# Kernel tuning notes

Hardware: AMD Instinct MI355X
Metric: run time of the kernel (lower is better)

Reference implementation:

```python
import jax, jax.numpy as jnp
import numpy as np

B, N, P, H, E, M, O, T = 16, 64, 192, 64, 32, 64, 64, 256

def _mlp(x, W1, b1, W2, b2):
    return jax.nn.relu(x @ W1 + b1) @ W2 + b2

def _qmul(q, r):
    w1, x1, y1, z1 = q[..., 0], q[..., 1], q[..., 2], q[..., 3]
    w2, x2, y2, z2 = r[..., 0], r[..., 1], r[..., 2], r[..., 3]
    return jnp.stack([
        w1*w2 - x1*x2 - y1*y2 - z1*z2,
        w1*x2 + x1*w2 + y1*z2 - z1*y2,
        w1*y2 - x1*z2 + y1*w2 + z1*x2,
        w1*z2 + x1*y2 - y1*x2 + z1*w2], axis=-1)

def _qrot(q, v):
    # rotate vector v by unit quaternion q (w,x,y,z)
    qv = q[..., 1:]
    t = 2.0 * jnp.cross(qv, v)
    return v + q[..., :1] * t + jnp.cross(qv, t)

def _normalize(x):
    return x / jnp.maximum(jnp.linalg.norm(x, axis=-1, keepdims=True), 1e-12)

def _lin(k, i, o, s=0.05):
    return jax.random.normal(k, (i, o), jnp.float32) * s

def setup_inputs():
    key = jax.random.key(0)
    ks = jax.random.split(key, 24)
    return dict(
        peptide_quats=_normalize(jax.random.normal(ks[0], (B, N, 4), jnp.float32)),
        peptide_trans=jax.random.normal(ks[1], (B, N, 3), jnp.float32) * 10.0,
        peptide_torsions=_normalize(jax.random.normal(ks[2], (B, N, 7, 2), jnp.float32)),
        peptide_feats=jax.random.normal(ks[3], (B, N, H), jnp.float32),
        edge_feats=jax.random.normal(ks[4], (B, N, N, E), jnp.float32),
        pocket_feats=jax.random.normal(ks[5], (B, P, H), jnp.float32),
        pocket_quats=_normalize(jax.random.normal(ks[6], (B, P, 4), jnp.float32)),
        pocket_trans=jax.random.normal(ks[7], (B, P, 3), jnp.float32) * 10.0,
        Wm1=_lin(ks[8], 2*H + E + 9, T), bm1=jnp.zeros((T,), jnp.float32),
        Wm2=_lin(ks[9], T, M), bm2=jnp.zeros((M,), jnp.float32),
        Wf1=_lin(ks[10], H + M, T), bf1=jnp.zeros((T,), jnp.float32),
        Wf2=_lin(ks[11], T, O), bf2=jnp.zeros((O,), jnp.float32),
        Wt1=_lin(ks[12], M, T), bt1=jnp.zeros((T,), jnp.float32),
        Wt2=_lin(ks[13], T, 3), bt2=jnp.zeros((3,), jnp.float32),
        Wq1=_lin(ks[14], M, T), bq1=jnp.zeros((T,), jnp.float32),
        Wq2=_lin(ks[15], T, 4), bq2=jnp.zeros((4,), jnp.float32),
        Wo1=_lin(ks[16], M + 14, T), bo1=jnp.zeros((T,), jnp.float32),
        Wo2=_lin(ks[17], T, 14), bo2=jnp.zeros((14,), jnp.float32),
        peptide_mask=jnp.ones((B, N), bool),
        pocket_mask=jnp.ones((B, P), bool),
    )

def reference(peptide_quats, peptide_trans, peptide_torsions, peptide_feats, edge_feats,
              pocket_feats, pocket_quats, pocket_trans,
              Wm1, bm1, Wm2, bm2, Wf1, bf1, Wf2, bf2, Wt1, bt1, Wt2, bt2,
              Wq1, bq1, Wq2, bq2, Wo1, bo1, Wo2, bo2, peptide_mask, pocket_mask):
    NP = N + P
    eye = jnp.eye(N, dtype=bool)
    pep_mm = peptide_mask[..., :, None] & peptide_mask[..., None, :] & ~eye
    poc_mm = peptide_mask[..., :, None] & pocket_mask[..., None, :]
    mm = jnp.concatenate([pep_mm, poc_mm], axis=-1)  # [B,N,N+P]

    all_q = jnp.concatenate([peptide_quats, pocket_quats], axis=-2)  # [B,N+P,4]
    all_x = jnp.concatenate([peptide_trans, pocket_trans], axis=-2)  # [B,N+P,3]

    conj = jnp.asarray([1.0, -1.0, -1.0, -1.0], peptide_quats.dtype)
    q_inv = all_q * conj                 # inverse rotation (unit quats)
    t_inv = -_qrot(q_inv, all_x)         # inverse translation

    # express peptide position i in the local frame of neighbour j
    local_x = _qrot(q_inv[..., None, :, :], peptide_trans[..., :, None, :]) + t_inv[..., None, :, :]
    local_q = _qmul(q_inv[..., None, :, :], peptide_quats[..., :, None, :])
    d2 = jnp.sum(jnp.square(peptide_trans[..., :, None, :] - all_x[..., None, :, :]), axis=-1)
    qdot = jnp.abs(jnp.sum(peptide_quats[..., :, None, :] * all_q[..., None, :, :], axis=-1))

    h_i = jnp.broadcast_to(peptide_feats[..., :, None, :], (B, N, NP, H))
    all_h = jnp.concatenate([peptide_feats, pocket_feats], axis=-2)
    h_j = jnp.broadcast_to(all_h[..., None, :, :], (B, N, NP, H))
    e = jnp.concatenate([edge_feats, jnp.zeros((B, N, P, E), edge_feats.dtype)], axis=-2)

    msg_in = jnp.concatenate([h_i, h_j, e, local_x, local_q, d2[..., None], qdot[..., None]], axis=-1)
    message = _mlp(msg_in, Wm1, bm1, Wm2, bm2) * mm[..., None]
    msg_sum = message.sum(axis=-2)  # [B,N,M]

    o = _mlp(jnp.concatenate([peptide_feats, msg_sum], axis=-1), Wf1, bf1, Wf2, bf2)

    n_msg = mm.sum(axis=-1).astype(message.dtype)
    c = jnp.where(n_msg > 0, 1.0 / jnp.maximum(n_msg, 1.0), 0.0)
    has_msg = n_msg > 0

    # translation update (rotate per-edge delta from neighbour local to global frame)
    delta_x = _mlp(message, Wt1, bt1, Wt2, bt2) * mm[..., None]
    rotated = _qrot(all_q[..., None, :, :], delta_x)
    upd_x = peptide_trans + rotated.sum(axis=-2) * c[..., None]

    # rotation update
    dq = _normalize(_mlp(msg_sum * c[..., None], Wq1, bq1, Wq2, bq2))
    upd_q = jnp.where(has_msg[..., None], _qmul(peptide_quats, dq), peptide_quats)
    upd_q = _normalize(upd_q)  # Rigid(..., normalize_quats=True)

    # torsion update (angle addition in sin/cos form)
    flat_t = peptide_torsions.reshape(B, N, 14)
    dt = _mlp(jnp.concatenate([msg_sum * c[..., None], flat_t], axis=-1), Wo1, bo1, Wo2, bo2)
    dt = _normalize(dt.reshape(B, N, 7, 2))
    s1, c1 = peptide_torsions[..., 0], peptide_torsions[..., 1]
    s2, c2 = dt[..., 0], dt[..., 1]
    mult = jnp.stack([s1 * c2 + c1 * s2, c1 * c2 - s1 * s2], axis=-1)
    upd_t = jnp.where(has_msg[..., None, None], mult, peptide_torsions)

    return upd_q, upd_x, upd_t, o
```

## Files before the change

### kernel.cpp

```cpp
#include <hip/hip_runtime.h>


typedef _Float16 f16;
typedef f16 f16x8 __attribute__((ext_vector_type(8)));
typedef f16 f16x4 __attribute__((ext_vector_type(4)));
typedef float f32x4 __attribute__((ext_vector_type(4)));
#define MFMA16(a, b, c) __builtin_amdgcn_mfma_f32_16x16x32_f16(a, b, c, 0, 0, 0)

#define B_ 16
#define N_ 64
#define P_ 192
#define NP_ 256
#define H_ 64
#define T_ 256

#define OFF_HIA    0
#define OFF_HJB    262144
#define OFF_B1T    1379328
#define OFF_W2T    1387520
#define OFF_WT1H   1395712
#define OFF_W1AT   1403904
#define OFF_W1BT   1412096

#define OUT_UPDQ 0
#define OUT_UPDX 4096
#define OUT_UPDT 7168
#define OUT_O    21504

__device__ __forceinline__ void qrot(float qw, float qx, float qy, float qz,
                                     float vx, float vy, float vz,
                                     float& ox, float& oy, float& oz) {
    float tx = 2.f * (qy * vz - qz * vy);
    float ty = 2.f * (qz * vx - qx * vz);
    float tz = 2.f * (qx * vy - qy * vx);
    ox = vx + qw * tx + (qy * tz - qz * ty);
    oy = vy + qw * ty + (qz * tx - qx * tz);
    oz = vz + qw * tz + (qx * ty - qy * tx);
}

struct Wts {
    const float *Wm1,*bm1,*Wm2,*bm2,*Wf1,*bf1,*Wf2,*bf2,*Wt1,*bt1,*Wt2,*bt2,
                *Wq1,*bq1,*Wq2,*bq2,*Wo1,*bo1,*Wo2,*bo2;
};

__global__ __launch_bounds__(256) void k_prep(const float* __restrict__ Wm1,
                                              const float* __restrict__ Wm2,
                                              const float* __restrict__ Wt1,
                                              float* __restrict__ ws) {
    int t = blockIdx.x * 256 + threadIdx.x;
    if (t < 16384) {
        f16* B1T = (f16*)(ws + OFF_B1T);
        int c = t >> 6, k = t & 63;
        float v = 0.f;
        if (k < 32) v = Wm1[(128 + k) * 256 + c];
        else if (k < 41) v = Wm1[(160 + (k - 32)) * 256 + c];
        B1T[t] = (f16)v;
    } else if (t < 32768) {
        f16* W2T = (f16*)(ws + OFF_W2T);
        int u = t - 16384;
        int m = u >> 8, c = u & 255;
        W2T[u] = (f16)Wm2[c * 64 + m];
    } else if (t < 49152) {
        f16* W1H = (f16*)(ws + OFF_WT1H);
        int u = t - 32768;
        int c = u >> 6, m = u & 63;
        W1H[u] = (f16)Wt1[m * 256 + c];
    } else if (t < 65536) {
        f16* W1A = (f16*)(ws + OFF_W1AT);
        int u = t - 49152;
        int c = u >> 6, k = u & 63;
        W1A[u] = (f16)Wm1[k * 256 + c];
    } else {
        f16* W1B = (f16*)(ws + OFF_W1BT);
        int u = t - 65536;
        int c = u >> 6, k = u & 63;
        W1B[u] = (f16)Wm1[(64 + k) * 256 + c];
    }
}

__global__ __launch_bounds__(256) void k_dots(const float* __restrict__ pep_h,
                                              const float* __restrict__ poc_h,
                                              float* __restrict__ ws) {
    const int ct = blockIdx.x;
    const int b = blockIdx.y;
    const int tid = threadIdx.x;
    const int lane = tid & 63;
    const int wv = tid >> 6;
    const int lm = lane & 15;
    const int lq = lane >> 4;

    __shared__ __align__(16) f16 hL[256 * 64];

    {
        const float4* p4 = (const float4*)(pep_h + (size_t)b * 4096);
        #pragma unroll
        for (int it = 0; it < 4; it++) {
            int idx = it * 256 + tid;
            float4 v = p4[idx];
            f16x4 h = {(f16)v.x, (f16)v.y, (f16)v.z, (f16)v.w};
            *(f16x4*)&hL[idx * 4] = h;
        }
        const float4* q4 = (const float4*)(poc_h + (size_t)b * 12288);
        #pragma unroll
        for (int it = 0; it < 12; it++) {
            int idx = it * 256 + tid;
            float4 v = q4[idx];
            f16x4 h = {(f16)v.x, (f16)v.y, (f16)v.z, (f16)v.w};
            *(f16x4*)&hL[4096 + idx * 4] = h;
        }
    }
    __syncthreads();

    const f16* W1AT = (const f16*)(ws + OFF_W1AT);
    const f16* W1BT = (const f16*)(ws + OFF_W1BT);

    f32x4 acc[4][4];
    #pragma unroll
    for (int mt = 0; mt < 4; mt++)
        #pragma unroll
        for (int nt = 0; nt < 4; nt++) acc[mt][nt] = (f32x4){0.f, 0.f, 0.f, 0.f};

    f16x8 af[4][2], bf[4][2];
    #pragma unroll
    for (int mt = 0; mt < 4; mt++) {
        const int c = ct * 64 + mt * 16 + lm;
        af[mt][0] = *(const f16x8*)&W1BT[c * 64 + lq * 8];
        af[mt][1] = *(const f16x8*)&W1BT[c * 64 + 32 + lq * 8];
    }
    #pragma unroll
    for (int nt = 0; nt < 4; nt++) {
        const int jj = wv * 64 + nt * 16 + lm;
        bf[nt][0] = *(const f16x8*)&hL[jj * 64 + lq * 8];
        bf[nt][1] = *(const f16x8*)&hL[jj * 64 + 32 + lq * 8];
    }
    #pragma unroll
    for (int mt = 0; mt < 4; mt++)
        #pragma unroll
        for (int nt = 0; nt < 4; nt++) {
            acc[mt][nt] = MFMA16(af[mt][0], bf[nt][0], acc[mt][nt]);
            acc[mt][nt] = MFMA16(af[mt][1], bf[nt][1], acc[mt][nt]);
        }
    float* HJ = ws + OFF_HJB + (size_t)b * 65536;
    #pragma unroll
    for (int mt = 0; mt < 4; mt++)
        #pragma unroll
        for (int nt = 0; nt < 4; nt++)
            #pragma unroll
            for (int r = 0; r < 4; r++)
                HJ[(size_t)(ct * 64 + mt * 16 + lq * 4 + r) * 256 +
                   wv * 64 + nt * 16 + lm] = acc[mt][nt][r];

    f32x4 ha[4];
    #pragma unroll
    for (int nt = 0; nt < 4; nt++) ha[nt] = (f32x4){0.f, 0.f, 0.f, 0.f};
    f16x8 a0 = *(const f16x8*)&hL[(wv * 16 + lm) * 64 + lq * 8];
    f16x8 a1 = *(const f16x8*)&hL[(wv * 16 + lm) * 64 + 32 + lq * 8];
    #pragma unroll
    for (int nt = 0; nt < 4; nt++) {
        const int c = ct * 64 + nt * 16 + lm;
        f16x8 b0 = *(const f16x8*)&W1AT[c * 64 + lq * 8];
        f16x8 b1 = *(const f16x8*)&W1AT[c * 64 + 32 + lq * 8];
        ha[nt] = MFMA16(a0, b0, ha[nt]);
        ha[nt] = MFMA16(a1, b1, ha[nt]);
    }
    #pragma unroll
    for (int nt = 0; nt < 4; nt++)
        #pragma unroll
        for (int r = 0; r < 4; r++)
            ws[OFF_HIA + (size_t)(b * 64 + wv * 16 + lq * 4 + r) * 256 +
               ct * 64 + nt * 16 + lm] = ha[nt][r];
}

__global__ __launch_bounds__(256, 2) void k_edge(const float* __restrict__ pep_q,
                                                 const float* __restrict__ pep_x,
                                                 const float* __restrict__ pep_t,
                                                 const float* __restrict__ pep_h,
                                                 const float* __restrict__ ef,
                                                 const float* __restrict__ poc_q,
                                                 const float* __restrict__ poc_x,
                                                 Wts W, float* __restrict__ ws,
                                                 float* __restrict__ out) {
    const int b = blockIdx.x & 15;
    const int i = blockIdx.x >> 4;
    const int node = b * 64 + i;
    const int tid = threadIdx.x;
    const int j = tid;
    const int lane = tid & 63;
    const int wv = tid >> 6;
    const int lm = lane & 15;
    const int lq = lane >> 4;
    const int j0w = wv * 64;
    const float cfac = 1.f / 255.f;

    __shared__ __align__(16) unsigned char RAW[45056];
    __shared__ float base_s[256], bt1s[256], wt2s[768];
    __shared__ float bm2s[64];
    __shared__ float msump[4][64];
    __shared__ float rotp[4][3];
    __shared__ float MS_s[64], MSC_s[64], ROT_s[3], DQ_s[4], DT_s[14];

    f16* const A1 = (f16*)RAW;
    f16* const Tw = (f16*)(RAW + 24576 + wv * 5120);
    float* const DXb = (float*)(RAW + 24576 + wv * 5120 + 2048);

    base_s[tid] = ws[OFF_HIA + (size_t)node * T_ + tid] + W.bm1[tid];
    bt1s[tid] = W.bt1[tid];
    if (tid < 64) bm2s[tid] = W.bm2[tid];
    wt2s[tid]       = W.Wt2[tid];
    wt2s[256 + tid] = W.Wt2[256 + tid];
    wt2s[512 + tid] = W.Wt2[512 + tid];

    const bool pep = (j < N_);
    {
        const float4 qi4 = *reinterpret_cast<const float4*>(pep_q + (b * N_ + i) * 4);
        const float qiw = qi4.x, qix = qi4.y, qiy = qi4.z, qiz = qi4.w;
        const float* tip = pep_x + (b * N_ + i) * 3;
        const float tix = tip[0], tiy = tip[1], tiz = tip[2];

        float qjw, qjx, qjy, qjz, xjx, xjy, xjz;
        if (pep) {
            const float4 q4 = *reinterpret_cast<const float4*>(pep_q + (b * N_ + j) * 4);
            qjw = q4.x; qjx = q4.y; qjy = q4.z; qjz = q4.w;
            const float* xp = pep_x + (b * N_ + j) * 3;
            xjx = xp[0]; xjy = xp[1]; xjz = xp[2];
        } else {
            const float4 q4 = *reinterpret_cast<const float4*>(poc_q + (b * P_ + (j - N_)) * 4);
            qjw = q4.x; qjx = q4.y; qjy = q4.z; qjz = q4.w;
            const float* xp = poc_x + (b * P_ + (j - N_)) * 3;
            xjx = xp[0]; xjy = xp[1]; xjz = xp[2];
        }

        const float vw = qjw, vx = -qjx, vy = -qjy, vz = -qjz;
        float tnx, tny, tnz;
        qrot(vw, vx, vy, vz, xjx, xjy, xjz, tnx, tny, tnz);
        float lxx, lxy, lxz;
        qrot(vw, vx, vy, vz, tix, tiy, tiz, lxx, lxy, lxz);
        lxx -= tnx; lxy -= tny; lxz -= tnz;
        float lqw = vw * qiw - vx * qix - vy * qiy - vz * qiz;
        float lqx = vw * qix + vx * qiw + vy * qiz - vz * qiy;
        float lqy = vw * qiy - vx * qiz + vy * qiw + vz * qix;
        float lqz = vw * qiz + vx * qiy - vy * qix + vz * qiw;
        float ddx = tix - xjx, ddy = tiy - xjy, ddz = tiz - xjz;
        float d2 = ddx * ddx + ddy * ddy + ddz * ddz;
        float qd = fabsf(qiw * qjw + qix * qjx + qiy * qjy + qiz * qjz);

        f16* arow = &A1[j * 48];
        const f16x8 z = {(f16)0,(f16)0,(f16)0,(f16)0,(f16)0,(f16)0,(f16)0,(f16)0};
        if (pep) {
            const float4* ep = reinterpret_cast<const float4*>(
                ef + (size_t)(((b * N_ + i) * N_) + j) * 32);
            #pragma unroll
            for (int gr = 0; gr < 4; gr++) {
                float4 v0 = ep[gr * 2], v1 = ep[gr * 2 + 1];
                f16x8 h;
                h[0]=(f16)v0.x; h[1]=(f16)v0.y; h[2]=(f16)v0.z; h[3]=(f16)v0.w;
                h[4]=(f16)v1.x; h[5]=(f16)v1.y; h[6]=(f16)v1.z; h[7]=(f16)v1.w;
                *(f16x8*)(arow + gr * 8) = h;
            }
        } else {
            #pragma unroll
            for (int gr = 0; gr < 4; gr++) *(f16x8*)(arow + gr * 8) = z;
        }
        f16x8 hg;
        hg[0]=(f16)lxx; hg[1]=(f16)lxy; hg[2]=(f16)lxz; hg[3]=(f16)lqw;
        hg[4]=(f16)lqx; hg[5]=(f16)lqy; hg[6]=(f16)lqz; hg[7]=(f16)d2;
        *(f16x8*)(arow + 32) = hg;
        f16x8 h2 = z; h2[0] = (f16)qd;
        *(f16x8*)(arow + 40) = h2;
    }
    __syncthreads();

    const f16* B1Tg = (const f16*)(ws + OFF_B1T);
    const f16* W2Tg = (const f16*)(ws + OFF_W2T);
    const f16* W1Hg = (const f16*)(ws + OFF_WT1H);
    const float* hjb = ws + OFF_HJB + (size_t)b * 65536;

    f32x4 msgacc[4][4];
    #pragma unroll
    for (int mt = 0; mt < 4; mt++)
        #pragma unroll
        for (int nt = 0; nt < 4; nt++)
            msgacc[mt][nt] = (f32x4){0.f, 0.f, 0.f, 0.f};

    const f16x8 zf = {(f16)0,(f16)0,(f16)0,(f16)0,(f16)0,(f16)0,(f16)0,(f16)0};

    f16x8 g1c[2][2], g2c[4], g1n[2][2], g2n[4];
    #pragma unroll
    for (int nt = 0; nt < 2; nt++) {
        const int c = nt * 16 + lm;
        g1c[nt][0] = *(const f16x8*)&B1Tg[c * 64 + lq * 8];
        g1c[nt][1] = *(const f16x8*)&B1Tg[c * 64 + 32 + lq * 8];
    }
    #pragma unroll
    for (int nt = 0; nt < 4; nt++)
        g2c[nt] = *(const f16x8*)&W2Tg[(nt * 16 + lm) * 256 + lq * 8];

    for (int ch = 0; ch < 8; ch++) {
        const int c0 = ch * 32;
        if (ch < 7) {
            const int c1 = c0 + 32;
            #pragma unroll
            for (int nt = 0; nt < 2; nt++) {
                const int c = c1 + nt * 16 + lm;
                g1n[nt][0] = *(const f16x8*)&B1Tg[c * 64 + lq * 8];
                g1n[nt][1] = *(const f16x8*)&B1Tg[c * 64 + 32 + lq * 8];
            }
            #pragma unroll
            for (int nt = 0; nt < 4; nt++)
                g2n[nt] = *(const f16x8*)&W2Tg[(nt * 16 + lm) * 256 + c1 + lq * 8];
        }
        float4 hv[4][2];
        #pragma unroll
        for (int mt = 0; mt < 4; mt++)
            #pragma unroll
            for (int nt = 0; nt < 2; nt++) {
                const int c = c0 + nt * 16 + lm;
                hv[mt][nt] = *(const float4*)&hjb[(size_t)c * 256 + j0w + mt * 16 + lq * 4];
            }
        #pragma unroll
        for (int mt = 0; mt < 4; mt++) {
            const int jr = j0w + mt * 16 + lm;
            f16x8 a0 = *(const f16x8*)&A1[jr * 48 + lq * 8];
            f16x8 a1 = zf;
            if (lq < 2) a1 = *(const f16x8*)&A1[jr * 48 + 32 + lq * 8];
            #pragma unroll
            for (int nt = 0; nt < 2; nt++) {
                const int c = c0 + nt * 16 + lm;
                f32x4 acc = {0.f, 0.f, 0.f, 0.f};
                acc = MFMA16(a0, g1c[nt][0], acc);
                acc = MFMA16(a1, g1c[nt][1], acc);
                const int jl = mt * 16 + lq * 4;
                const float bc = base_s[c];
                const float* hvp = (const float*)&hv[mt][nt];
                #pragma unroll
                for (int r = 0; r < 4; r++) {
                    float u = acc[r] + hvp[r] + bc;
                    u = fmaxf(u, 0.f);
                    Tw[(jl + r) * 40 + nt * 16 + lm] = (f16)u;
                }
            }
        }
        __builtin_amdgcn_wave_barrier();
        #pragma unroll
        for (int mt = 0; mt < 4; mt++) {
            f16x8 a0 = *(const f16x8*)&Tw[(mt * 16 + lm) * 40 + lq * 8];
            #pragma unroll
            for (int nt = 0; nt < 4; nt++)
                msgacc[mt][nt] = MFMA16(a0, g2c[nt], msgacc[mt][nt]);
        }
        __builtin_amdgcn_wave_barrier();
        #pragma unroll
        for (int nt = 0; nt < 2; nt++) { g1c[nt][0] = g1n[nt][0]; g1c[nt][1] = g1n[nt][1]; }
        #pragma unroll
        for (int nt = 0; nt < 4; nt++) g2c[nt] = g2n[nt];
    }

    float sums[4] = {0.f, 0.f, 0.f, 0.f};
    #pragma unroll
    for (int mt = 0; mt < 4; mt++) {
        f16* bandrow = (mt < 3) ? (f16*)(RAW + wv * 6144 + (mt * 16) * 128)
                                : (f16*)(RAW + 24576 + wv * 5120);
        #pragma unroll
        for (int nt = 0; nt < 4; nt++) {
            const int m = nt * 16 + lm;
            f32x4 a = msgacc[mt][nt];
            #pragma unroll
            for (int r = 0; r < 4; r++) {
                const int jj = j0w + mt * 16 + lq * 4 + r;
                float v = a[r] + bm2s[m];
                if (jj == i) v = 0.f;
                bandrow[(lq * 4 + r) * 64 + m] = (f16)v;
                sums[nt] += v;
            }
        }
    }
    #pragma unroll
    for (int nt = 0; nt < 4; nt++) {
        float s = sums[nt];
        s += __shfl_xor(s, 16);
        s += __shfl_xor(s, 32);
        if (lane < 16) msump[wv][nt * 16 + lane] = s;
    }
    __syncthreads();
    if (tid < 64) {
        float s = msump[0][tid] + msump[1][tid] + msump[2][tid] + msump[3][tid];
        MS_s[tid] = s; MSC_s[tid] = s * cfac;
    }

    #pragma unroll
    for (int mt = 0; mt < 4; mt++) {
        const f16* mrow = (mt < 3)
            ? (const f16*)(RAW + wv * 6144 + (mt * 16 + lm) * 128)
            : (const f16*)(RAW + 24576 + wv * 5120 + lm * 128);
        f16x8 a0 = *(const f16x8*)&mrow[lq * 8];
        f16x8 a1 = *(const f16x8*)&mrow[32 + lq * 8];
        float d0[4] = {0,0,0,0}, d1[4] = {0,0,0,0}, d2a[4] = {0,0,0,0};
        #pragma unroll 8
        for (int nt = 0; nt < 16; nt++) {
            const int c = nt * 16 + lm;
            f16x8 b0 = *(const f16x8*)&W1Hg[c * 64 + lq * 8];
            f16x8 b1 = *(const f16x8*)&W1Hg[c * 64 + 32 + lq * 8];
            f32x4 acc = {0.f, 0.f, 0.f, 0.f};
            acc = MFMA16(a0, b0, acc);
            acc = MFMA16(a1, b1, acc);
            const float w0 = wt2s[c * 3 + 0];
            const float w1 = wt2s[c * 3 + 1];
            const float w2 = wt2s[c * 3 + 2];
            const float bc = bt1s[c];
            #pragma unroll
            for (int r = 0; r < 4; r++) {
                float s = fmaxf(acc[r] + bc, 0.f);
                d0[r] = fmaf(s, w0, d0[r]);
                d1[r] = fmaf(s, w1, d1[r]);
                d2a[r] = fmaf(s, w2, d2a[r]);
            }
        }
        #pragma unroll
        for (int r = 0; r < 4; r++) {
            float v0 = d0[r], v1 = d1[r], v2 = d2a[r];
            v0 += __shfl_xor(v0, 1); v0 += __shfl_xor(v0, 2);
            v0 += __shfl_xor(v0, 4); v0 += __shfl_xor(v0, 8);
            v1 += __shfl_xor(v1, 1); v1 += __shfl_xor(v1, 2);
            v1 += __shfl_xor(v1, 4); v1 += __shfl_xor(v1, 8);
            v2 += __shfl_xor(v2, 1); v2 += __shfl_xor(v2, 2);
            v2 += __shfl_xor(v2, 4); v2 += __shfl_xor(v2, 8);
            if (lm == 0) {
                const int jl = mt * 16 + lq * 4 + r;
                DXb[jl * 3 + 0] = v0;
                DXb[jl * 3 + 1] = v1;
                DXb[jl * 3 + 2] = v2;
            }
        }
    }

    float qjw, qjx, qjy, qjz;
    {
        const float* qp = pep ? (pep_q + (b * N_ + j) * 4)
                              : (poc_q + (b * P_ + (j - N_)) * 4);
        const float4 q4 = *reinterpret_cast<const float4*>(qp);
        qjw = q4.x; qjx = q4.y; qjy = q4.z; qjz = q4.w;
    }
    const float maskf = (pep && j == i) ? 0.f : 1.f;
    float dx0 = (DXb[lane * 3 + 0] + W.bt2[0]) * maskf;
    float dx1 = (DXb[lane * 3 + 1] + W.bt2[1]) * maskf;
    float dx2 = (DXb[lane * 3 + 2] + W.bt2[2]) * maskf;
    float rx, ry, rz;
    qrot(qjw, qjx, qjy, qjz, dx0, dx1, dx2, rx, ry, rz);
    {
        float v = rx;
        v += __shfl_xor(v, 32); v += __shfl_xor(v, 16); v += __shfl_xor(v, 8);
        v += __shfl_xor(v, 4);  v += __shfl_xor(v, 2);  v += __shfl_xor(v, 1);
        if (lane == 0) rotp[wv][0] = v;
        v = ry;
        v += __shfl_xor(v, 32); v += __shfl_xor(v, 16); v += __shfl_xor(v, 8);
        v += __shfl_xor(v, 4);  v += __shfl_xor(v, 2);  v += __shfl_xor(v, 1);
        if (lane == 0) rotp[wv][1] = v;
        v = rz;
        v += __shfl_xor(v, 32); v += __shfl_xor(v, 16); v += __shfl_xor(v, 8);
        v += __shfl_xor(v, 4);  v += __shfl_xor(v, 2);  v += __shfl_xor(v, 1);
        if (lane == 0) rotp[wv][2] = v;
    }
    __syncthreads();

    float* const FB = (float*)RAW;
    float* const HIS  = FB;
    float* const TORs = FB + 64;
    float* const HB   = FB + 128;
    float* const HB2  = FB + 384;
    float* const HB3  = FB + 640;

    if (tid >= 64 && tid < 67) {
        int k = tid - 64;
        ROT_s[k] = rotp[0][k] + rotp[1][k] + rotp[2][k] + rotp[3][k];
    }
    if (tid < 64) HIS[tid] = pep_h[(size_t)node * 64 + tid];
    if (tid >= 96 && tid < 110) TORs[tid - 96] = pep_t[(size_t)node * 14 + (tid - 96)];
    __syncthreads();

    {
        float acc = W.bf1[tid];
        #pragma unroll 16
        for (int k = 0; k < 64; k++) acc = fmaf(HIS[k], W.Wf1[k * 256 + tid], acc);
        #pragma unroll 16
        for (int k = 0; k < 64; k++) acc = fmaf(MS_s[k], W.Wf1[(64 + k) * 256 + tid], acc);
        HB[tid] = fmaxf(acc, 0.f);
    }
    __syncthreads();
    {
        float p = 0.f;
        #pragma unroll 16
        for (int c = 0; c < 64; c++)
            p = fmaf(HB[wv * 64 + c], W.Wf2[(wv * 64 + c) * 64 + lane], p);
        msump[wv][lane] = p;
    }
    {
        float acc = W.bq1[tid];
        #pragma unroll 16
        for (int k = 0; k < 64; k++) acc = fmaf(MSC_s[k], W.Wq1[k * 256 + tid], acc);
        HB2[tid] = fmaxf(acc, 0.f);
    }
    {
        float acc = W.bo1[tid];
        #pragma unroll 16
        for (int k = 0; k < 64; k++) acc = fmaf(MSC_s[k], W.Wo1[k * 256 + tid], acc);
        #pragma unroll
        for (int k = 0; k < 14; k++) acc = fmaf(TORs[k], W.Wo1[(64 + k) * 256 + tid], acc);
        HB3[tid] = fmaxf(acc, 0.f);
    }
    __syncthreads();
    if (tid < 64) {
        float o = W.bf2[tid] + msump[0][tid] + msump[1][tid] + msump[2][tid] + msump[3][tid];
        out[OUT_O + (size_t)node * 64 + tid] = o;
    }
    {
        float p = 0.f;
        #pragma unroll
        for (int t4 = 0; t4 < 4; t4++) {
            int c = t4 * 64 + lane;
            p = fmaf(HB2[c], W.Wq2[c * 4 + wv], p);
        }
        p += __shfl_xor(p, 32); p += __shfl_xor(p, 16); p += __shfl_xor(p, 8);
        p += __shfl_xor(p, 4);  p += __shfl_xor(p, 2);  p += __shfl_xor(p, 1);
        if (lane == 0) DQ_s[wv] = p + W.bq2[wv];
    }
    {
        const int g = tid >> 4, l16 = tid & 15;
        if (g < 14) {
            float p = 0.f;
            #pragma unroll
            for (int t16 = 0; t16 < 16; t16++) {
                int c = t16 * 16 + l16;
                p = fmaf(HB3[c], W.Wo2[c * 14 + g], p);
            }
            p += __shfl_xor(p, 8); p += __shfl_xor(p, 4);
            p += __shfl_xor(p, 2); p += __shfl_xor(p, 1);
            if (l16 == 0) DT_s[g] = p + W.bo2[g];
        }
    }
    __syncthreads();

    if (tid == 0) {
        float w_ = DQ_s[0], x_ = DQ_s[1], y_ = DQ_s[2], z_ = DQ_s[3];
        float n = fmaxf(sqrtf(w_ * w_ + x_ * x_ + y_ * y_ + z_ * z_), 1e-12f);
        w_ /= n; x_ /= n; y_ /= n; z_ /= n;
        const float4 qi4 = *reinterpret_cast<const float4*>(pep_q + (size_t)node * 4);
        float aw = qi4.x, ax = qi4.y, ay = qi4.z, az = qi4.w;
        float uw = aw * w_ - ax * x_ - ay * y_ - az * z_;
        float ux = aw * x_ + ax * w_ + ay * z_ - az * y_;
        float uy = aw * y_ - ax * z_ + ay * w_ + az * x_;
        float uz = aw * z_ + ax * y_ - ay * x_ + az * w_;
        float n2 = fmaxf(sqrtf(uw * uw + ux * ux + uy * uy + uz * uz), 1e-12f);
        out[OUT_UPDQ + (size_t)node * 4 + 0] = uw / n2;
        out[OUT_UPDQ + (size_t)node * 4 + 1] = ux / n2;
        out[OUT_UPDQ + (size_t)node * 4 + 2] = uy / n2;
        out[OUT_UPDQ + (size_t)node * 4 + 3] = uz / n2;
    }
    if (tid >= 32 && tid < 35) {
        int k = tid - 32;
        out[OUT_UPDX + (size_t)node * 3 + k] =
            pep_x[(size_t)node * 3 + k] + ROT_s[k] * cfac;
    }
    if (tid >= 48 && tid < 55) {
        int t = tid - 48;
        float s2 = DT_s[2 * t], c2 = DT_s[2 * t + 1];
        float n = fmaxf(sqrtf(s2 * s2 + c2 * c2), 1e-12f);
        s2 /= n; c2 /= n;
        float s1 = TORs[2 * t], c1 = TORs[2 * t + 1];
        out[OUT_UPDT + (size_t)node * 14 + 2 * t]     = s1 * c2 + c1 * s2;
        out[OUT_UPDT + (size_t)node * 14 + 2 * t + 1] = c1 * c2 - s1 * s2;
    }
}

extern "C" void kernel_launch(void* const* d_in, const int* in_sizes, int n_in,
                              void* d_out, int out_size, void* d_ws, size_t ws_size,
                              hipStream_t stream) {
    (void)in_sizes; (void)n_in; (void)out_size; (void)ws_size;
    const float* pep_q = (const float*)d_in[0];
    const float* pep_x = (const float*)d_in[1];
    const float* pep_t = (const float*)d_in[2];
    const float* pep_h = (const float*)d_in[3];
    const float* ef    = (const float*)d_in[4];
    const float* poc_h = (const float*)d_in[5];
    const float* poc_q = (const float*)d_in[6];
    const float* poc_x = (const float*)d_in[7];
    float* ws = (float*)d_ws;
    float* out = (float*)d_out;

    Wts W;
    W.Wm1 = (const float*)d_in[8];  W.bm1 = (const float*)d_in[9];
    W.Wm2 = (const float*)d_in[10]; W.bm2 = (const float*)d_in[11];
    W.Wf1 = (const float*)d_in[12]; W.bf1 = (const float*)d_in[13];
    W.Wf2 = (const float*)d_in[14]; W.bf2 = (const float*)d_in[15];
    W.Wt1 = (const float*)d_in[16]; W.bt1 = (const float*)d_in[17];
    W.Wt2 = (const float*)d_in[18]; W.bt2 = (const float*)d_in[19];
    W.Wq1 = (const float*)d_in[20]; W.bq1 = (const float*)d_in[21];
    W.Wq2 = (const float*)d_in[22]; W.bq2 = (const float*)d_in[23];
    W.Wo1 = (const float*)d_in[24]; W.bo1 = (const float*)d_in[25];
    W.Wo2 = (const float*)d_in[26]; W.bo2 = (const float*)d_in[27];

    k_prep<<<320, 256, 0, stream>>>(W.Wm1, W.Wm2, W.Wt1, ws);
    k_dots<<<dim3(4, 16), 256, 0, stream>>>(pep_h, poc_h, ws);
    k_edge<<<1024, 256, 0, stream>>>(pep_q, pep_x, pep_t, pep_h, ef,
                                     poc_q, poc_x, W, ws, out);
}
```

Measured before the change: 269.5 us.

## Use 512-thread blocks in k_edge with 32 edges per wave

Doubles the k_edge block to 8 waves, so each wave handles 32 neighbour edges instead of 64. The per-wave shared-memory scratch layout and the reductions are remapped to fit, and the node-level MLP tail is split across the two halves of the block. The aim is more waves in flight to hide latency and a shorter per-wave serial chain. In exchange, the weight fragments each wave loads from global memory are amortised over fewer edges, and the block needs more registers and barriers.

```diff
diff --git a/kernel.cpp b/kernel.cpp
--- a/kernel.cpp
+++ b/kernel.cpp
@@ -171,7 +171,7 @@
                ct * 64 + nt * 16 + lm] = ha[nt][r];
 }
 
-__global__ __launch_bounds__(256, 2) void k_edge(const float* __restrict__ pep_q,
+__global__ __launch_bounds__(512, 4) void k_edge(const float* __restrict__ pep_q,
                                                  const float* __restrict__ pep_x,
                                                  const float* __restrict__ pep_t,
                                                  const float* __restrict__ pep_h,
@@ -184,34 +184,35 @@
     const int i = blockIdx.x >> 4;
     const int node = b * 64 + i;
     const int tid = threadIdx.x;
-    const int j = tid;
     const int lane = tid & 63;
     const int wv = tid >> 6;
     const int lm = lane & 15;
     const int lq = lane >> 4;
-    const int j0w = wv * 64;
+    const int j0w = wv * 32;
     const float cfac = 1.f / 255.f;
 
     __shared__ __align__(16) unsigned char RAW[45056];
     __shared__ float base_s[256], bt1s[256], wt2s[768];
     __shared__ float bm2s[64];
-    __shared__ float msump[4][64];
-    __shared__ float rotp[4][3];
+    __shared__ float msump[8][64];
+    __shared__ float rotp[8][3];
     __shared__ float MS_s[64], MSC_s[64], ROT_s[3], DQ_s[4], DT_s[14];
 
     f16* const A1 = (f16*)RAW;
-    f16* const Tw = (f16*)(RAW + 24576 + wv * 5120);
-    float* const DXb = (float*)(RAW + 24576 + wv * 5120 + 2048);
-
-    base_s[tid] = ws[OFF_HIA + (size_t)node * T_ + tid] + W.bm1[tid];
-    bt1s[tid] = W.bt1[tid];
-    if (tid < 64) bm2s[tid] = W.bm2[tid];
-    wt2s[tid]       = W.Wt2[tid];
-    wt2s[256 + tid] = W.Wt2[256 + tid];
-    wt2s[512 + tid] = W.Wt2[512 + tid];
-
-    const bool pep = (j < N_);
-    {
+    f16* const Tw = (f16*)(RAW + 24576 + wv * 2560);
+    float* const DXb = (float*)(RAW + 24576 + wv * 2560 + 1024);
+
+    if (tid >= 256) {
+        const int t2 = tid - 256;
+        base_s[t2] = ws[OFF_HIA + (size_t)node * T_ + t2] + W.bm1[t2];
+        bt1s[t2] = W.bt1[t2];
+        wt2s[t2]       = W.Wt2[t2];
+        wt2s[256 + t2] = W.Wt2[256 + t2];
+        if (t2 < 64) bm2s[t2] = W.bm2[t2];
+    } else {
+        wt2s[512 + tid] = W.Wt2[512 + tid];
+        const int j = tid;
+        const bool pep = (j < N_);
         const float4 qi4 = *reinterpret_cast<const float4*>(pep_q + (b * N_ + i) * 4);
         const float qiw = qi4.x, qix = qi4.y, qiy = qi4.z, qiz = qi4.w;
         const float* tip = pep_x + (b * N_ + i) * 3;
@@ -275,9 +276,9 @@
     const f16* W1Hg = (const f16*)(ws + OFF_WT1H);
     const float* hjb = ws + OFF_HJB + (size_t)b * 65536;
 
-    f32x4 msgacc[4][4];
-    #pragma unroll
-    for (int mt = 0; mt < 4; mt++)
+    f32x4 msgacc[2][4];
+    #pragma unroll
+    for (int mt = 0; mt < 2; mt++)
         #pragma unroll
         for (int nt = 0; nt < 4; nt++)
             msgacc[mt][nt] = (f32x4){0.f, 0.f, 0.f, 0.f};
@@ -309,16 +310,16 @@
             for (int nt = 0; nt < 4; nt++)
                 g2n[nt] = *(const f16x8*)&W2Tg[(nt * 16 + lm) * 256 + c1 + lq * 8];
         }
-        float4 hv[4][2];
-        #pragma unroll
-        for (int mt = 0; mt < 4; mt++)
+        float4 hv[2][2];
+        #pragma unroll
+        for (int mt = 0; mt < 2; mt++)
             #pragma unroll
             for (int nt = 0; nt < 2; nt++) {
                 const int c = c0 + nt * 16 + lm;
                 hv[mt][nt] = *(const float4*)&hjb[(size_t)c * 256 + j0w + mt * 16 + lq * 4];
             }
         #pragma unroll
-        for (int mt = 0; mt < 4; mt++) {
+        for (int mt = 0; mt < 2; mt++) {
             const int jr = j0w + mt * 16 + lm;
             f16x8 a0 = *(const f16x8*)&A1[jr * 48 + lq * 8];
             f16x8 a1 = zf;
@@ -342,7 +343,7 @@
         }
         __builtin_amdgcn_wave_barrier();
         #pragma unroll
-        for (int mt = 0; mt < 4; mt++) {
+        for (int mt = 0; mt < 2; mt++) {
             f16x8 a0 = *(const f16x8*)&Tw[(mt * 16 + lm) * 40 + lq * 8];
             #pragma unroll
             for (int nt = 0; nt < 4; nt++)
@@ -357,19 +358,21 @@
 
     float sums[4] = {0.f, 0.f, 0.f, 0.f};
     #pragma unroll
-    for (int mt = 0; mt < 4; mt++) {
-        f16* bandrow = (mt < 3) ? (f16*)(RAW + wv * 6144 + (mt * 16) * 128)
-                                : (f16*)(RAW + 24576 + wv * 5120);
+    for (int mt = 0; mt < 2; mt++) {
         #pragma unroll
         for (int nt = 0; nt < 4; nt++) {
             const int m = nt * 16 + lm;
             f32x4 a = msgacc[mt][nt];
             #pragma unroll
             for (int r = 0; r < 4; r++) {
-                const int jj = j0w + mt * 16 + lq * 4 + r;
+                const int lrow = mt * 16 + lq * 4 + r;
+                const int jj = j0w + lrow;
                 float v = a[r] + bm2s[m];
                 if (jj == i) v = 0.f;
-                bandrow[(lq * 4 + r) * 64 + m] = (f16)v;
+                f16* rowp = (lrow < 24)
+                    ? (f16*)(RAW + wv * 3072) + lrow * 64
+                    : (f16*)(RAW + 24576 + wv * 2560) + (lrow - 24) * 64;
+                rowp[m] = (f16)v;
                 sums[nt] += v;
             }
         }
@@ -383,15 +386,18 @@
     }
     __syncthreads();
     if (tid < 64) {
-        float s = msump[0][tid] + msump[1][tid] + msump[2][tid] + msump[3][tid];
+        float s = 0.f;
+        #pragma unroll
+        for (int w = 0; w < 8; w++) s += msump[w][tid];
         MS_s[tid] = s; MSC_s[tid] = s * cfac;
     }
 
     #pragma unroll
-    for (int mt = 0; mt < 4; mt++) {
-        const f16* mrow = (mt < 3)
-            ? (const f16*)(RAW + wv * 6144 + (mt * 16 + lm) * 128)
-            : (const f16*)(RAW + 24576 + wv * 5120 + lm * 128);
+    for (int mt = 0; mt < 2; mt++) {
+        const int lrow = mt * 16 + lm;
+        const f16* mrow = (lrow < 24)
+            ? (const f16*)(RAW + wv * 3072) + lrow * 64
+            : (const f16*)(RAW + 24576 + wv * 2560) + (lrow - 24) * 64;
         f16x8 a0 = *(const f16x8*)&mrow[lq * 8];
         f16x8 a1 = *(const f16x8*)&mrow[32 + lq * 8];
         float d0[4] = {0,0,0,0}, d1[4] = {0,0,0,0}, d2a[4] = {0,0,0,0};
@@ -433,20 +439,20 @@
         }
     }
 
-    float qjw, qjx, qjy, qjz;
     {
-        const float* qp = pep ? (pep_q + (b * N_ + j) * 4)
-                              : (poc_q + (b * P_ + (j - N_)) * 4);
+        const int jloc = lane & 31;
+        const int j4 = j0w + jloc;
+        const bool pep4 = (j4 < N_);
+        const float* qp = pep4 ? (pep_q + (b * N_ + j4) * 4)
+                               : (poc_q + (b * P_ + (j4 - N_)) * 4);
         const float4 q4 = *reinterpret_cast<const float4*>(qp);
-        qjw = q4.x; qjx = q4.y; qjy = q4.z; qjz = q4.w;
-    }
-    const float maskf = (pep && j == i) ? 0.f : 1.f;
-    float dx0 = (DXb[lane * 3 + 0] + W.bt2[0]) * maskf;
-    float dx1 = (DXb[lane * 3 + 1] + W.bt2[1]) * maskf;
-    float dx2 = (DXb[lane * 3 + 2] + W.bt2[2]) * maskf;
-    float rx, ry, rz;
-    qrot(qjw, qjx, qjy, qjz, dx0, dx1, dx2, rx, ry, rz);
-    {
+        const float maskf = (pep4 && j4 == i) ? 0.f : 1.f;
+        float dx0 = (DXb[jloc * 3 + 0] + W.bt2[0]) * maskf;
+        float dx1 = (DXb[jloc * 3 + 1] + W.bt2[1]) * maskf;
+        float dx2 = (DXb[jloc * 3 + 2] + W.bt2[2]) * maskf;
+        float rx, ry, rz;
+        qrot(q4.x, q4.y, q4.z, q4.w, dx0, dx1, dx2, rx, ry, rz);
+        if (lane >= 32) { rx = 0.f; ry = 0.f; rz = 0.f; }
         float v = rx;
         v += __shfl_xor(v, 32); v += __shfl_xor(v, 16); v += __shfl_xor(v, 8);
         v += __shfl_xor(v, 4);  v += __shfl_xor(v, 2);  v += __shfl_xor(v, 1);
@@ -471,48 +477,53 @@
 
     if (tid >= 64 && tid < 67) {
         int k = tid - 64;
-        ROT_s[k] = rotp[0][k] + rotp[1][k] + rotp[2][k] + rotp[3][k];
+        float s = 0.f;
+        #pragma unroll
+        for (int w = 0; w < 8; w++) s += rotp[w][k];
+        ROT_s[k] = s;
     }
     if (tid < 64) HIS[tid] = pep_h[(size_t)node * 64 + tid];
     if (tid >= 96 && tid < 110) TORs[tid - 96] = pep_t[(size_t)node * 14 + (tid - 96)];
     __syncthreads();
 
-    {
+    if (tid < 256) {
         float acc = W.bf1[tid];
         #pragma unroll 16
         for (int k = 0; k < 64; k++) acc = fmaf(HIS[k], W.Wf1[k * 256 + tid], acc);
         #pragma unroll 16
         for (int k = 0; k < 64; k++) acc = fmaf(MS_s[k], W.Wf1[(64 + k) * 256 + tid], acc);
         HB[tid] = fmaxf(acc, 0.f);
-    }
-    __syncthreads();
-    {
-        float p = 0.f;
+    } else {
+        const int m = tid - 256;
+        float acc = W.bq1[m];
         #pragma unroll 16
-        for (int c = 0; c < 64; c++)
-            p = fmaf(HB[wv * 64 + c], W.Wf2[(wv * 64 + c) * 64 + lane], p);
-        msump[wv][lane] = p;
-    }
-    {
-        float acc = W.bq1[tid];
-        #pragma unroll 16
-        for (int k = 0; k < 64; k++) acc = fmaf(MSC_s[k], W.Wq1[k * 256 + tid], acc);
-        HB2[tid] = fmaxf(acc, 0.f);
-    }
-    {
+        for (int k = 0; k < 64; k++) acc = fmaf(MSC_s[k], W.Wq1[k * 256 + m], acc);
+        HB2[m] = fmaxf(acc, 0.f);
+    }
+    __syncthreads();
+
+    if (tid < 256) {
         float acc = W.bo1[tid];
         #pragma unroll 16
         for (int k = 0; k < 64; k++) acc = fmaf(MSC_s[k], W.Wo1[k * 256 + tid], acc);
         #pragma unroll
         for (int k = 0; k < 14; k++) acc = fmaf(TORs[k], W.Wo1[(64 + k) * 256 + tid], acc);
         HB3[tid] = fmaxf(acc, 0.f);
-    }
-    __syncthreads();
+    } else {
+        const int w4 = wv - 4;
+        float p = 0.f;
+        #pragma unroll 16
+        for (int cc = 0; cc < 64; cc++)
+            p = fmaf(HB[w4 * 64 + cc], W.Wf2[(w4 * 64 + cc) * 64 + lane], p);
+        msump[w4][lane] = p;
+    }
+    __syncthreads();
+
     if (tid < 64) {
         float o = W.bf2[tid] + msump[0][tid] + msump[1][tid] + msump[2][tid] + msump[3][tid];
         out[OUT_O + (size_t)node * 64 + tid] = o;
     }
-    {
+    if (wv < 4) {
         float p = 0.f;
         #pragma unroll
         for (int t4 = 0; t4 < 4; t4++) {
@@ -522,9 +533,8 @@
         p += __shfl_xor(p, 32); p += __shfl_xor(p, 16); p += __shfl_xor(p, 8);
         p += __shfl_xor(p, 4);  p += __shfl_xor(p, 2);  p += __shfl_xor(p, 1);
         if (lane == 0) DQ_s[wv] = p + W.bq2[wv];
-    }
-    {
-        const int g = tid >> 4, l16 = tid & 15;
+    } else {
+        const int g = (tid - 256) >> 4, l16 = tid & 15;
         if (g < 14) {
             float p = 0.f;
             #pragma unroll
@@ -600,6 +610,6 @@
 
     k_prep<<<320, 256, 0, stream>>>(W.Wm1, W.Wm2, W.Wt1, ws);
     k_dots<<<dim3(4, 16), 256, 0, stream>>>(pep_h, poc_h, ws);
-    k_edge<<<1024, 256, 0, stream>>>(pep_q, pep_x, pep_t, pep_h, ef,
+    k_edge<<<1024, 512, 0, stream>>>(pep_q, pep_x, pep_t, pep_h, ef,
                                      poc_q, poc_x, W, ws, out);
 }
```

New measurement: 328.1 us. 1.22x slower.
